# Optimization experiments

Hardware: AMD Instinct MI355X
Metric: run time of the kernel (lower is better)

The kernel has to match this reference:

```python
import jax, jax.numpy as jnp
import numpy as np

B, T, DIM = 4, 1024, 2048
N_HEADS, N_KV_HEADS = 32, 8
HEAD_DIM = DIM // N_HEADS  # 64
N_REPS = N_HEADS // N_KV_HEADS  # 4


def setup_inputs() -> dict:
    key = jax.random.key(0)
    ks = jax.random.split(key, 8)
    # RoPE tables: theta = 10000^{-2i/d}, positions 0..T-1
    inv_freq = 1.0 / (10000.0 ** (jnp.arange(0, HEAD_DIM, 2, dtype=jnp.float32) / HEAD_DIM))
    angles = jnp.arange(T, dtype=jnp.float32)[:, None] * inv_freq[None, :]  # (T, HEAD_DIM//2)
    s = 0.02
    return {
        "input": jax.random.normal(ks[0], (B, T, DIM), jnp.float32),
        "freqs_cos": jnp.cos(angles),
        "freqs_sin": jnp.sin(angles),
        "mask": jnp.tril(jnp.ones((T, T), dtype=bool)),  # causal boolean mask
        "wq": s * jax.random.normal(ks[1], (DIM, DIM), jnp.float32),
        "wk": s * jax.random.normal(ks[2], (N_KV_HEADS * HEAD_DIM, DIM), jnp.float32),
        "wv": s * jax.random.normal(ks[3], (N_KV_HEADS * HEAD_DIM, DIM), jnp.float32),
        "wo": s * jax.random.normal(ks[4], (DIM, DIM), jnp.float32),
        "curr_pos": 0,
    }


def _apply_rope(x, cos, sin):
    # x: (B, T, H, D); cos/sin: (T, D//2). Complex multiply on (even, odd) pairs.
    xr = x[..., 0::2]
    xi = x[..., 1::2]
    c = cos[None, :, None, :]
    s = sin[None, :, None, :]
    out_r = xr * c - xi * s
    out_i = xr * s + xi * c
    return jnp.stack([out_r, out_i], axis=-1).reshape(x.shape)


def reference(input, freqs_cos, freqs_sin, mask, wq, wk, wv, wo, curr_pos):
    Bv, Tv = input.shape[0], input.shape[1]
    qs = (input @ wq.T).reshape(Bv, Tv, N_HEADS, HEAD_DIM)
    ks = (input @ wk.T).reshape(Bv, Tv, N_KV_HEADS, HEAD_DIM)
    vs = (input @ wv.T).reshape(Bv, Tv, N_KV_HEADS, HEAD_DIM)
    qs = _apply_rope(qs, freqs_cos, freqs_sin)
    ks = _apply_rope(ks, freqs_cos, freqs_sin)

    # KV cache (prefill path: curr_pos == 0, fresh cache of length 2T)
    kv_cache = jnp.zeros((Bv, 2 * Tv, N_KV_HEADS, HEAD_DIM, 2), input.dtype)
    kv_cache = kv_cache.at[:, curr_pos:curr_pos + Tv, :, :, 0].set(ks)
    kv_cache = kv_cache.at[:, curr_pos:curr_pos + Tv, :, :, 1].set(vs)
    k_all = kv_cache[:, :curr_pos + Tv, :, :, 0]
    v_all = kv_cache[:, :curr_pos + Tv, :, :, 1]

    # GQA: broadcast each kv head across its query-head group (avoid repeat_interleave copy)
    S = k_all.shape[1]
    q = qs.transpose(0, 2, 1, 3).reshape(Bv, N_KV_HEADS, N_REPS, Tv, HEAD_DIM)
    k = k_all.transpose(0, 2, 1, 3)  # (B, KVH, S, D)
    v = v_all.transpose(0, 2, 1, 3)

    scale = 1.0 / jnp.sqrt(jnp.asarray(HEAD_DIM, input.dtype))
    scores = jnp.einsum("bgrqd,bgkd->bgrqk", q, k) * scale  # (B, KVH, REPS, T, S)
    neg = jnp.asarray(jnp.finfo(input.dtype).min, input.dtype)
    scores = jnp.where(mask[None, None, None, :, :S], scores, neg)
    attn = jax.nn.softmax(scores, axis=-1)
    out = jnp.einsum("bgrqk,bgkd->bgrqd", attn, v)
    out = out.reshape(Bv, N_HEADS, Tv, HEAD_DIM).transpose(0, 2, 1, 3).reshape(Bv, Tv, DIM)
    return out @ wo.T
```

## Files before the change

### kernel.cpp

```cpp
#include <hip/hip_runtime.h>
#include <cstdint>

typedef __bf16 bf16x8 __attribute__((ext_vector_type(8)));
typedef float  f32x4  __attribute__((ext_vector_type(4)));
typedef float  f32x16 __attribute__((ext_vector_type(16)));
typedef float  float8v __attribute__((ext_vector_type(8)));
typedef unsigned short ushort8v __attribute__((ext_vector_type(8)));
typedef unsigned short ushort4v __attribute__((ext_vector_type(4)));
typedef unsigned int   uint4v   __attribute__((ext_vector_type(4)));

__device__ __forceinline__ unsigned short f2b(float f) {
  uint32_t u = __builtin_bit_cast(uint32_t, f);
  u += 0x7FFFu + ((u >> 16) & 1u);
  return (unsigned short)(u >> 16);
}
__device__ __forceinline__ float b2f(unsigned short h) {
  uint32_t u = ((uint32_t)h) << 16;
  return __builtin_bit_cast(float, u);
}
__device__ __forceinline__ unsigned int cvtpk(float lo, float hi_) {
  unsigned int r;
  asm("v_cvt_pk_bf16_f32 %0, %1, %2" : "=v"(r) : "v"(lo), "v"(hi_));
  return r;
}

__device__ __forceinline__ void async16(const void* g, void* l) {
  __builtin_amdgcn_global_load_lds(
      (const __attribute__((address_space(1))) void*)g,
      (__attribute__((address_space(3))) void*)l, 16, 0, 0);
}

#define WAITVM(N)  __builtin_amdgcn_s_waitcnt(0x0F70 | ((N) & 15))

struct CvtArgs {
  const float* src[5];
  unsigned short* dst[5];
  long n[5];
};
__global__ void cvt5_kernel(CvtArgs a) {
  long base = (long)blockIdx.x * blockDim.x + threadIdx.x;
  long gstride = (long)gridDim.x * blockDim.x;
#pragma unroll 1
  for (int sg = 0; sg < 5; ++sg) {
    const float* s = a.src[sg];
    unsigned short* d = a.dst[sg];
    long n8 = a.n[sg] >> 3;
    for (long i = base; i < n8; i += gstride) {
      float8v f = *(const float8v*)(s + i * 8);
      ushort8v o;
#pragma unroll
      for (int j = 0; j < 8; ++j) o[j] = f2b(f[j]);
      *(ushort8v*)(d + i * 8) = o;
    }
  }
}

template<bool F32OUT, int BM, int BN, int GX, int GY>
__global__ __launch_bounds__(512, 2)
void gemm2ph(const unsigned short* __restrict__ Ag, const unsigned short* __restrict__ Wg,
             void* __restrict__ Cp, int N) {
  constexpr int K = 2048;
  constexpr int MF = BM / 32;
  constexpr int NF = BN / 64;
  constexpr int AL = BM / 128;
  constexpr int BL = BN / 128;
  constexpr int IPP = AL + BL;
  constexpr int ASLOT = BM * 64;
  constexpr int BSLOT = BN * 64;
  constexpr int NWG = GX * GY;
  constexpr int CPX = NWG / 8;

  extern __shared__ char lds_c[];

  const int tid = threadIdx.x;
  const int wave = tid >> 6, lane = tid & 63;
  const int wm = wave >> 2, wn = wave & 3;
  const int lr = lane & 15, lg = lane >> 4;

  const int flat = blockIdx.y * GX + blockIdx.x;
  const int swz = (flat & 7) * CPX + (flat >> 3);
  const int m0 = (swz / GX) * BM, n0 = (swz % GX) * BN;

  const int laneSw = (lr >> 1) * 128 + (((((lr & 1) << 2) | lg) ^ (lr >> 1)) << 4);
  const int aoff = wm * (BM / 2) * 64 + laneSw;
  const int boff = wn * NF * 1024 + laneSw;

  f32x4 acc[MF][NF] = {};

  auto stageA = [&](int s) {
    char* slot = lds_c + (s & 3) * ASLOT;
    const int kc = s * 32;
#pragma unroll
    for (int j = 0; j < AL; ++j) {
      int q = (tid + 512 * j) * 16;
      int R = q >> 7, g2L = ((q >> 4) & 7) ^ (R & 7);
      int row = R * 2 + (g2L >> 2), kg = g2L & 3;
      async16(Ag + (size_t)(m0 + row) * K + kc + kg * 8, slot + q);
    }
  };
  auto stageB = [&](int s) {
    char* slot = lds_c + 4 * ASLOT + (s & 3) * BSLOT;
    const int kc = s * 32;
#pragma unroll
    for (int j = 0; j < BL; ++j) {
      int q = (tid + 512 * j) * 16;
      int R = q >> 7, g2L = ((q >> 4) & 7) ^ (R & 7);
      int row = R * 2 + (g2L >> 2), kg = g2L & 3;
      async16(Wg + (size_t)(n0 + row) * K + kc + kg * 8, slot + q);
    }
  };

#define PH(P, VM, DOST)                                                       \
  {                                                                           \
    __builtin_amdgcn_sched_barrier(0);                                        \
    const char* As_ = lds_c + ((P) & 3) * ASLOT;                              \
    const char* Bs_ = lds_c + 4 * ASLOT + ((P) & 3) * BSLOT;                  \
    bf16x8 af_[MF], bf_[NF];                                                  \
    _Pragma("unroll") for (int mi = 0; mi < MF; ++mi)                         \
      af_[mi] = *(const bf16x8*)(As_ + aoff + mi * 1024);                     \
    _Pragma("unroll") for (int ni = 0; ni < NF; ++ni)                         \
      bf_[ni] = *(const bf16x8*)(Bs_ + boff + ni * 1024);                     \
    if (DOST) { stageA((P) + 3); stageB((P) + 3); }                           \
    WAITVM(VM);                                                               \
    __builtin_amdgcn_s_barrier();                                             \
    __builtin_amdgcn_s_setprio(1);                                            \
    _Pragma("unroll") for (int mi = 0; mi < MF; ++mi)                         \
      _Pragma("unroll") for (int ni = 0; ni < NF; ++ni)                       \
        acc[mi][ni] = __builtin_amdgcn_mfma_f32_16x16x32_bf16(                \
            af_[mi], bf_[ni], acc[mi][ni], 0, 0, 0);                          \
    __builtin_amdgcn_s_setprio(0);                                            \
    __builtin_amdgcn_s_barrier();                                             \
  }

  stageA(0); stageB(0);
  stageA(1); stageB(1);
  stageA(2); stageB(2);
  WAITVM(2 * IPP);
  __builtin_amdgcn_s_barrier();

  for (int p2 = 0; p2 < 60; p2 += 4) {
    PH(p2 + 0, 2 * IPP, true);
    PH(p2 + 1, 2 * IPP, true);
    PH(p2 + 2, 2 * IPP, true);
    PH(p2 + 3, 2 * IPP, true);
  }
  PH(60, 2 * IPP, true);
  PH(61, IPP, false);
  PH(62, 0, false);
  PH(63, 0, false);
#undef PH

#pragma unroll
  for (int mig = 0; mig < MF; ++mig) {
#pragma unroll
    for (int j = 0; j < 4; ++j) {
      int row = m0 + wm * (BM / 2) + mig * 16 + lg * 4 + j;
#pragma unroll
      for (int ni = 0; ni < NF; ++ni) {
        int col = n0 + wn * (NF * 16) + ni * 16 + lr;
        float v = acc[mig][ni][j];
        if (F32OUT) ((float*)Cp)[(size_t)row * N + col] = v;
        else        ((unsigned short*)Cp)[(size_t)row * N + col] = f2b(v);
      }
    }
  }
}

__global__ __launch_bounds__(256)
void ropekv_kernel(unsigned short* __restrict__ qkv,
                   const float* __restrict__ cosb, const float* __restrict__ sinb,
                   unsigned short* __restrict__ vt) {
  const int tt0 = blockIdx.x * 64;
  const int kvh = blockIdx.y;
  const int b   = blockIdx.z;
  const int tid = threadIdx.x;

  {
    int r = tid >> 2, c0 = (tid & 3) * 16;
    int t = tt0 + r;
    unsigned short* kp = qkv + (size_t)(b * 1024 + t) * 3072 + 2048 + kvh * 64 + c0;
    const float* cb = cosb + t * 32 + c0 / 2;
    const float* sb = sinb + t * 32 + c0 / 2;
    ushort8v x0 = *(const ushort8v*)kp;
    ushort8v x1 = *(const ushort8v*)(kp + 8);
    float8v c = *(const float8v*)cb;
    float8v s = *(const float8v*)sb;
    ushort8v o0, o1;
#pragma unroll
    for (int j = 0; j < 4; ++j) {
      float xr = b2f(x0[2 * j]), xi = b2f(x0[2 * j + 1]);
      o0[2 * j]     = f2b(xr * c[j] - xi * s[j]);
      o0[2 * j + 1] = f2b(xr * s[j] + xi * c[j]);
    }
#pragma unroll
    for (int j = 0; j < 4; ++j) {
      float xr = b2f(x1[2 * j]), xi = b2f(x1[2 * j + 1]);
      o1[2 * j]     = f2b(xr * c[4 + j] - xi * s[4 + j]);
      o1[2 * j + 1] = f2b(xr * s[4 + j] + xi * c[4 + j]);
    }
    *(ushort8v*)kp = o0;
    *(ushort8v*)(kp + 8) = o1;
  }

  __shared__ unsigned short lT[64 * 68];
#pragma unroll
  for (int i = 0; i < 2; ++i) {
    int r = i * 32 + (tid >> 3), c = (tid & 7) * 8;
    const unsigned short* src = qkv + (size_t)(b * 1024 + tt0 + r) * 3072 + 2560 + kvh * 64 + c;
    ushort8v v = *(const ushort8v*)src;
    ushort4v a, b4;
#pragma unroll
    for (int j = 0; j < 4; ++j) { a[j] = v[j]; b4[j] = v[j + 4]; }
    *(ushort4v*)&lT[r * 68 + c]     = a;
    *(ushort4v*)&lT[r * 68 + c + 4] = b4;
  }
  __syncthreads();
#pragma unroll
  for (int i = 0; i < 2; ++i) {
    int d = tid & 63;
    int tt = i * 4 + (tid >> 6);
    ushort8v o;
#pragma unroll
    for (int j = 0; j < 8; ++j) o[j] = lT[(tt * 8 + j) * 68 + d];
    *(ushort8v*)&vt[((size_t)((b * 8 + kvh) * 64 + d)) * 1024 + tt0 + tt * 8] = o;
  }
}

__global__ __launch_bounds__(256, 2)
void attn_kernel(const unsigned short* __restrict__ qkv, const unsigned short* __restrict__ vt,
                 const float* __restrict__ cosb, const float* __restrict__ sinb,
                 unsigned short* __restrict__ ob) {
  const int flat = (blockIdx.z * 8 + blockIdx.y) * 16 + blockIdx.x;
  const int swzb = (flat & 7) * 64 + (flat >> 3);
  const int bx = swzb & 15, kvh = (swzb >> 4) & 7, b = swzb >> 7;

  const int tid = threadIdx.x, wave = tid >> 6, lane = tid & 63;
  const int l31 = lane & 31, hi = lane >> 5;
  const int h = kvh * 4 + wave;

  const int qth = 31 - bx, qtl = bx;
  const int q0h = qth * 32, q0l = qtl * 32;
  const int nth = qth / 4 + 1, ntl = qtl / 4 + 1;
  const int ntot = nth + ntl;

  __shared__ unsigned short lK[2][128 * 64];
  __shared__ unsigned short lVt[2][64 * 128];

  auto ldq = [&](int q0, bf16x8* qf) {
    int t = q0 + l31;
    const unsigned short* qp = qkv + (size_t)(b * 1024 + t) * 3072 + h * 64;
#pragma unroll
    for (int dk = 0; dk < 4; ++dk) {
      ushort8v q = *(const ushort8v*)(qp + dk * 16 + hi * 8);
      f32x4 c4 = *(const f32x4*)(cosb + t * 32 + dk * 8 + hi * 4);
      f32x4 s4 = *(const f32x4*)(sinb + t * 32 + dk * 8 + hi * 4);
      ushort8v o;
#pragma unroll
      for (int j = 0; j < 4; ++j) {
        float xr = b2f(q[2 * j]), xi = b2f(q[2 * j + 1]);
        o[2 * j]     = f2b(xr * c4[j] - xi * s4[j]);
        o[2 * j + 1] = f2b(xr * s4[j] + xi * c4[j]);
      }
      qf[dk] = __builtin_bit_cast(bf16x8, o);
    }
  };

  const unsigned short* kg = qkv + (size_t)(b * 1024) * 3072 + 2048 + kvh * 64;
  const unsigned short* vg = vt + (size_t)(b * 8 + kvh) * 64 * 1024;

  auto stage = [&](int kvb, int bi) {
    const int sr  = tid >> 3;
    const int scb = (tid & 7) * 16;
#pragma unroll
    for (int i = 0; i < 4; ++i) {
      int r = i * 32 + sr;
      int cb = scb ^ ((r & 7) << 4);
      async16(kg + (size_t)(kvb + r) * 3072 + (cb >> 1), &lK[bi][r * 64 + (scb >> 1)]);
    }
    const int rv0 = tid >> 4;
    const int scv = (tid & 15) * 16;
#pragma unroll
    for (int i = 0; i < 4; ++i) {
      int rv = i * 16 + rv0;
      int cbv = scv ^ ((rv & 15) << 4);
      async16(vg + (size_t)rv * 1024 + kvb + (cbv >> 1), &lVt[bi][rv * 128 + (scv >> 1)]);
    }
  };

  bf16x8 qf[4];
  f32x16 oacc[2] = {};
  float m2 = -3e38f, l_run = 0.f;
  int q0 = q0h;

  ldq(q0h, qf);

  const float SC = 0.125f * 1.44269504f;

  auto chunk64 = [&](int cur, int ckvb, int c, bool lastT) {
    f32x16 sd[2] = {};
    __builtin_amdgcn_s_setprio(1);
#pragma unroll
    for (int s = 0; s < 2; ++s) {
      const int krow = c * 64 + s * 32 + l31;
      const char* kr = (const char*)lK[cur] + krow * 128;
      const int swz = (krow & 7) << 4;
#pragma unroll
      for (int dk = 0; dk < 4; ++dk) {
        bf16x8 kf = *(const bf16x8*)(kr + ((dk * 32 + hi * 16) ^ swz));
        sd[s] = __builtin_amdgcn_mfma_f32_32x32x16_bf16(kf, qf[dk], sd[s], 0, 0, 0);
      }
    }
    __builtin_amdgcn_s_setprio(0);

#pragma unroll
    for (int s = 0; s < 2; ++s)
#pragma unroll
      for (int r = 0; r < 16; ++r) {
        float v = sd[s][r] * SC;
        if (lastT) {
          int kvg = ckvb + s * 32 + (r & 3) + 8 * (r >> 2) + 4 * hi;
          if (kvg > q0 + l31) v = -3e38f;
        }
        sd[s][r] = v;
      }
    float pm = sd[0][0];
#pragma unroll
    for (int s = 0; s < 2; ++s)
#pragma unroll
      for (int r = 0; r < 16; ++r) pm = fmaxf(pm, sd[s][r]);
    pm = fmaxf(pm, __shfl_xor(pm, 32));
    if (!__all(pm <= m2 + 11.0f)) {
      float mnew = fmaxf(m2, pm);
      float alpha = exp2f(m2 - mnew);
      m2 = mnew;
      l_run *= alpha;
#pragma unroll
      for (int db = 0; db < 2; ++db)
#pragma unroll
        for (int r = 0; r < 16; ++r) oacc[db][r] *= alpha;
    }
    float tsum = 0.f;
#pragma unroll
    for (int s = 0; s < 2; ++s)
#pragma unroll
      for (int r = 0; r < 16; ++r) { float p = exp2f(sd[s][r] - m2); sd[s][r] = p; tsum += p; }
    tsum += __shfl_xor(tsum, 32);
    l_run += tsum;

    bf16x8 pf[2][2];
#pragma unroll
    for (int s = 0; s < 2; ++s)
#pragma unroll
      for (int kc = 0; kc < 2; ++kc) {
        unsigned int cA = cvtpk(sd[s][8 * kc + 0], sd[s][8 * kc + 1]);
        unsigned int cB = cvtpk(sd[s][8 * kc + 4], sd[s][8 * kc + 5]);
        unsigned int cC = cvtpk(sd[s][8 * kc + 2], sd[s][8 * kc + 3]);
        unsigned int cD = cvtpk(sd[s][8 * kc + 6], sd[s][8 * kc + 7]);
        unsigned int xA = __shfl_xor(cA, 32), xB = __shfl_xor(cB, 32);
        unsigned int xC = __shfl_xor(cC, 32), xD = __shfl_xor(cD, 32);
        uint4v u;
        u[0] = hi ? xB : cA;
        u[1] = hi ? xD : cC;
        u[2] = hi ? cB : xA;
        u[3] = hi ? cD : xC;
        pf[s][kc] = __builtin_bit_cast(bf16x8, u);
      }

    __builtin_amdgcn_s_setprio(1);
#pragma unroll
    for (int db = 0; db < 2; ++db) {
      const int row = db * 32 + l31;
      const char* vr = (const char*)lVt[cur] + row * 256;
      const int vswz = (row & 15) << 4;
#pragma unroll
      for (int s = 0; s < 2; ++s)
#pragma unroll
        for (int kc = 0; kc < 2; ++kc) {
          bf16x8 vf = *(const bf16x8*)(vr + ((c * 128 + s * 64 + kc * 32 + hi * 16) ^ vswz));
          oacc[db] = __builtin_amdgcn_mfma_f32_32x32x16_bf16(vf, pf[s][kc], oacc[db], 0, 0, 0);
        }
    }
    __builtin_amdgcn_s_setprio(0);
  };

  auto writeOut = [&](int q0w) {
    float inv = 1.0f / l_run;
    unsigned short* orow = ob + (size_t)(b * 1024 + q0w + l31) * 2048 + h * 64;
#pragma unroll
    for (int db = 0; db < 2; ++db)
#pragma unroll
      for (int g = 0; g < 4; ++g) {
        int d0 = db * 32 + 8 * g + 4 * hi;
        ushort4v o;
#pragma unroll
        for (int j = 0; j < 4; ++j) o[j] = f2b(oacc[db][4 * g + j] * inv);
        *(ushort4v*)(orow + d0) = o;
      }
  };

  auto kvb_of = [&](int j) { return (j < nth ? j : j - nth) * 128; };

  stage(0, 0);
  __syncthreads();

  for (int j = 0; j < ntot; ++j) {
    const int cur = j & 1;
    if (j + 1 < ntot) stage(kvb_of(j + 1), cur ^ 1);
    const int kvb = kvb_of(j);
    const bool lastT = (j == nth - 1) || (j == ntot - 1);

#pragma unroll 1
    for (int c = 0; c < 2; ++c) {
      if (kvb + c * 64 > q0 + 31) continue;
      chunk64(cur, kvb + c * 64, c, lastT);
    }

    if (j == nth - 1) {
      writeOut(q0h);
      oacc[0] = f32x16{}; oacc[1] = f32x16{};
      m2 = -3e38f; l_run = 0.f;
      q0 = q0l;
      ldq(q0l, qf);
    }
    __syncthreads();
  }
  writeOut(q0l);
}

extern "C" void kernel_launch(void* const* d_in, const int* in_sizes, int n_in,
                              void* d_out, int out_size, void* d_ws, size_t ws_size,
                              hipStream_t stream) {
  const float* input = (const float*)d_in[0];
  const float* fcos  = (const float*)d_in[1];
  const float* fsin  = (const float*)d_in[2];
  const float* wq = (const float*)d_in[4];
  const float* wk = (const float*)d_in[5];
  const float* wv = (const float*)d_in[6];
  const float* wo = (const float*)d_in[7];
  float* out = (float*)d_out;

  unsigned short* xb   = (unsigned short*)d_ws;
  unsigned short* wqkv = xb + (size_t)4096 * 2048;
  unsigned short* wob  = wqkv + (size_t)3072 * 2048;
  unsigned short* qkv  = wob + (size_t)2048 * 2048;
  unsigned short* ob   = qkv + (size_t)4096 * 3072;
  unsigned short* vtb  = xb;

  hipFuncSetAttribute((const void*)&gemm2ph<false, 256, 256, 12, 16>,
                      hipFuncAttributeMaxDynamicSharedMemorySize, 131072);
  hipFuncSetAttribute((const void*)&gemm2ph<true, 128, 256, 8, 32>,
                      hipFuncAttributeMaxDynamicSharedMemorySize, 98304);

  CvtArgs ca;
  ca.src[0] = input; ca.dst[0] = xb;                        ca.n[0] = (long)4096 * 2048;
  ca.src[1] = wq;    ca.dst[1] = wqkv;                      ca.n[1] = (long)2048 * 2048;
  ca.src[2] = wk;    ca.dst[2] = wqkv + (size_t)2048 * 2048; ca.n[2] = (long)512 * 2048;
  ca.src[3] = wv;    ca.dst[3] = wqkv + (size_t)2560 * 2048; ca.n[3] = (long)512 * 2048;
  ca.src[4] = wo;    ca.dst[4] = wob;                       ca.n[4] = (long)2048 * 2048;
  hipLaunchKernelGGL(cvt5_kernel, dim3(2048), dim3(256), 0, stream, ca);

  hipLaunchKernelGGL((gemm2ph<false, 256, 256, 12, 16>), dim3(12, 16), dim3(512), 131072,
                     stream, xb, wqkv, (void*)qkv, 3072);

  hipLaunchKernelGGL(ropekv_kernel, dim3(16, 8, 4), dim3(256), 0, stream,
                     qkv, fcos, fsin, vtb);

  hipLaunchKernelGGL(attn_kernel, dim3(16, 8, 4), dim3(256), 0, stream,
                     qkv, vtb, fcos, fsin, ob);

  hipLaunchKernelGGL((gemm2ph<true, 128, 256, 8, 32>), dim3(8, 32), dim3(512), 98304,
                     stream, ob, wob, (void*)out, 2048);
}
```

Measured before the change: 171.8 us.

## Split GEMM k-steps into 8 half-phases with staggered A/B staging

Rewrites the bf16 GEMM mainloop so each k-step is split into two half-phases over M halves. A fragments are reloaded per half and B fragments are reused across both. Global-to-LDS staging of A and B is interleaved one chunk per half-phase, and the vmcnt wait happens only every other step. The output-projection GEMM changes from BM=128/BN=256 tiles to BM=256/BN=128 tiles. The aim is finer-grained overlap of loads with MFMA and less LDS read pressure, at the cost of twice as many barriers and a larger accumulator footprint.

```diff
diff --git a/kernel.cpp b/kernel.cpp
--- a/kernel.cpp
+++ b/kernel.cpp
@@ -55,16 +55,16 @@
   }
 }
 
-template<bool F32OUT, int BM, int BN, int GX, int GY>
+template<bool F32OUT, int BN, int GX, int GY>
 __global__ __launch_bounds__(512, 2)
-void gemm2ph(const unsigned short* __restrict__ Ag, const unsigned short* __restrict__ Wg,
-             void* __restrict__ Cp, int N) {
+void gemm8p(const unsigned short* __restrict__ Ag, const unsigned short* __restrict__ Wg,
+            void* __restrict__ Cp, int N) {
   constexpr int K = 2048;
-  constexpr int MF = BM / 32;
+  constexpr int BM = 256;
   constexpr int NF = BN / 64;
-  constexpr int AL = BM / 128;
+  constexpr int AL = 2;
   constexpr int BL = BN / 128;
-  constexpr int IPP = AL + BL;
+  constexpr int VMS = 2 * BL + AL;
   constexpr int ASLOT = BM * 64;
   constexpr int BSLOT = BN * 64;
   constexpr int NWG = GX * GY;
@@ -82,79 +82,87 @@
   const int m0 = (swz / GX) * BM, n0 = (swz % GX) * BN;
 
   const int laneSw = (lr >> 1) * 128 + (((((lr & 1) << 2) | lg) ^ (lr >> 1)) << 4);
-  const int aoff = wm * (BM / 2) * 64 + laneSw;
+  const int aoff = wm * 128 * 64 + laneSw;
   const int boff = wn * NF * 1024 + laneSw;
 
-  f32x4 acc[MF][NF] = {};
-
-  auto stageA = [&](int s) {
-    char* slot = lds_c + (s & 3) * ASLOT;
+  f32x4 acc[8][NF] = {};
+  bf16x8 af[4], bf[NF];
+
+  auto stA = [&](int slot, int s) {
+    char* sl = lds_c + slot * ASLOT;
     const int kc = s * 32;
 #pragma unroll
     for (int j = 0; j < AL; ++j) {
       int q = (tid + 512 * j) * 16;
       int R = q >> 7, g2L = ((q >> 4) & 7) ^ (R & 7);
       int row = R * 2 + (g2L >> 2), kg = g2L & 3;
-      async16(Ag + (size_t)(m0 + row) * K + kc + kg * 8, slot + q);
-    }
-  };
-  auto stageB = [&](int s) {
-    char* slot = lds_c + 4 * ASLOT + (s & 3) * BSLOT;
+      async16(Ag + (size_t)(m0 + row) * K + kc + kg * 8, sl + q);
+    }
+  };
+  auto stB = [&](int slot, int s) {
+    char* sl = lds_c + 4 * ASLOT + slot * BSLOT;
     const int kc = s * 32;
 #pragma unroll
     for (int j = 0; j < BL; ++j) {
       int q = (tid + 512 * j) * 16;
       int R = q >> 7, g2L = ((q >> 4) & 7) ^ (R & 7);
       int row = R * 2 + (g2L >> 2), kg = g2L & 3;
-      async16(Wg + (size_t)(n0 + row) * K + kc + kg * 8, slot + q);
-    }
-  };
-
-#define PH(P, VM, DOST)                                                       \
+      async16(Wg + (size_t)(n0 + row) * K + kc + kg * 8, sl + q);
+    }
+  };
+
+#define PH(RSLOT, MH, RDB, STG, VM)                                           \
   {                                                                           \
-    __builtin_amdgcn_sched_barrier(0);                                        \
-    const char* As_ = lds_c + ((P) & 3) * ASLOT;                              \
-    const char* Bs_ = lds_c + 4 * ASLOT + ((P) & 3) * BSLOT;                  \
-    bf16x8 af_[MF], bf_[NF];                                                  \
-    _Pragma("unroll") for (int mi = 0; mi < MF; ++mi)                         \
-      af_[mi] = *(const bf16x8*)(As_ + aoff + mi * 1024);                     \
-    _Pragma("unroll") for (int ni = 0; ni < NF; ++ni)                         \
-      bf_[ni] = *(const bf16x8*)(Bs_ + boff + ni * 1024);                     \
-    if (DOST) { stageA((P) + 3); stageB((P) + 3); }                           \
-    WAITVM(VM);                                                               \
+    const char* As_ = lds_c + (RSLOT) * ASLOT;                                \
+    _Pragma("unroll") for (int mi = 0; mi < 4; ++mi)                          \
+      af[mi] = *(const bf16x8*)(As_ + aoff + ((MH) * 4 + mi) * 1024);         \
+    if (RDB) {                                                                \
+      const char* Bs_ = lds_c + 4 * ASLOT + (RSLOT) * BSLOT;                  \
+      _Pragma("unroll") for (int ni = 0; ni < NF; ++ni)                       \
+        bf[ni] = *(const bf16x8*)(Bs_ + boff + ni * 1024);                    \
+    }                                                                         \
+    STG;                                                                      \
+    if ((VM) >= 0) WAITVM(VM);                                                \
     __builtin_amdgcn_s_barrier();                                             \
     __builtin_amdgcn_s_setprio(1);                                            \
-    _Pragma("unroll") for (int mi = 0; mi < MF; ++mi)                         \
+    _Pragma("unroll") for (int mi = 0; mi < 4; ++mi)                          \
       _Pragma("unroll") for (int ni = 0; ni < NF; ++ni)                       \
-        acc[mi][ni] = __builtin_amdgcn_mfma_f32_16x16x32_bf16(                \
-            af_[mi], bf_[ni], acc[mi][ni], 0, 0, 0);                          \
+        acc[(MH) * 4 + mi][ni] = __builtin_amdgcn_mfma_f32_16x16x32_bf16(     \
+            af[mi], bf[ni], acc[(MH) * 4 + mi][ni], 0, 0, 0);                 \
     __builtin_amdgcn_s_setprio(0);                                            \
     __builtin_amdgcn_s_barrier();                                             \
   }
 
-  stageA(0); stageB(0);
-  stageA(1); stageB(1);
-  stageA(2); stageB(2);
-  WAITVM(2 * IPP);
+  stB(0, 0); stA(0, 0); stB(1, 1); stA(1, 1); stB(2, 2); stA(2, 2); stB(3, 3);
+  WAITVM(VMS);
   __builtin_amdgcn_s_barrier();
 
-  for (int p2 = 0; p2 < 60; p2 += 4) {
-    PH(p2 + 0, 2 * IPP, true);
-    PH(p2 + 1, 2 * IPP, true);
-    PH(p2 + 2, 2 * IPP, true);
-    PH(p2 + 3, 2 * IPP, true);
-  }
-  PH(60, 2 * IPP, true);
-  PH(61, IPP, false);
-  PH(62, 0, false);
-  PH(63, 0, false);
+  for (int T = 0; T < 30; T += 2) {
+    const int p0 = 2 * T;
+    PH(0, 0, true,  stA(3, p0 + 3), -1);
+    PH(0, 1, false, stB(0, p0 + 4), -1);
+    PH(1, 0, true,  stA(0, p0 + 4), -1);
+    PH(1, 1, false, stB(1, p0 + 5), VMS);
+    PH(2, 0, true,  stA(1, p0 + 5), -1);
+    PH(2, 1, false, stB(2, p0 + 6), -1);
+    PH(3, 0, true,  stA(2, p0 + 6), -1);
+    PH(3, 1, false, stB(3, p0 + 7), VMS);
+  }
+  PH(0, 0, true,  stA(3, 63), -1);
+  PH(0, 1, false, (void)0, -1);
+  PH(1, 0, true,  (void)0, -1);
+  PH(1, 1, false, (void)0, 0);
+  PH(2, 0, true,  (void)0, -1);
+  PH(2, 1, false, (void)0, -1);
+  PH(3, 0, true,  (void)0, -1);
+  PH(3, 1, false, (void)0, -1);
 #undef PH
 
 #pragma unroll
-  for (int mig = 0; mig < MF; ++mig) {
+  for (int mig = 0; mig < 8; ++mig) {
 #pragma unroll
     for (int j = 0; j < 4; ++j) {
-      int row = m0 + wm * (BM / 2) + mig * 16 + lg * 4 + j;
+      int row = m0 + wm * 128 + mig * 16 + lg * 4 + j;
 #pragma unroll
       for (int ni = 0; ni < NF; ++ni) {
         int col = n0 + wn * (NF * 16) + ni * 16 + lr;
@@ -446,9 +454,9 @@
   unsigned short* ob   = qkv + (size_t)4096 * 3072;
   unsigned short* vtb  = xb;
 
-  hipFuncSetAttribute((const void*)&gemm2ph<false, 256, 256, 12, 16>,
+  hipFuncSetAttribute((const void*)&gemm8p<false, 256, 12, 16>,
                       hipFuncAttributeMaxDynamicSharedMemorySize, 131072);
-  hipFuncSetAttribute((const void*)&gemm2ph<true, 128, 256, 8, 32>,
+  hipFuncSetAttribute((const void*)&gemm8p<true, 128, 16, 16>,
                       hipFuncAttributeMaxDynamicSharedMemorySize, 98304);
 
   CvtArgs ca;
@@ -459,7 +467,7 @@
   ca.src[4] = wo;    ca.dst[4] = wob;                       ca.n[4] = (long)2048 * 2048;
   hipLaunchKernelGGL(cvt5_kernel, dim3(2048), dim3(256), 0, stream, ca);
 
-  hipLaunchKernelGGL((gemm2ph<false, 256, 256, 12, 16>), dim3(12, 16), dim3(512), 131072,
+  hipLaunchKernelGGL((gemm8p<false, 256, 12, 16>), dim3(12, 16), dim3(512), 131072,
                      stream, xb, wqkv, (void*)qkv, 3072);
 
   hipLaunchKernelGGL(ropekv_kernel, dim3(16, 8, 4), dim3(256), 0, stream,
@@ -468,6 +476,6 @@
   hipLaunchKernelGGL(attn_kernel, dim3(16, 8, 4), dim3(256), 0, stream,
                      qkv, vtb, fcos, fsin, ob);
 
-  hipLaunchKernelGGL((gemm2ph<true, 128, 256, 8, 32>), dim3(8, 32), dim3(512), 98304,
+  hipLaunchKernelGGL((gemm8p<true, 128, 16, 16>), dim3(16, 16), dim3(512), 98304,
                      stream, ob, wob, (void*)out, 2048);
 }
```

New measurement: 168.3 us. 1.02x faster.
